# Kernel tuning notes

Hardware: AMD Instinct MI355X
Metric: run time of the kernel (lower is better)

Reference implementation:

```python
import jax, jax.numpy as jnp
import numpy as np

B, T, C, H = 2, 2048, 1024, 16
Dh = C // H  # 64
EPS = 1e-5


def layer_norm(x, g, b):
    mu = jnp.mean(x, axis=-1, keepdims=True)
    var = jnp.mean(jnp.square(x - mu), axis=-1, keepdims=True)
    return (x - mu) * jax.lax.rsqrt(var + EPS) * g + b


def setup_inputs() -> dict:
    key = jax.random.key(0)
    ks = jax.random.split(key, 12)
    s = 0.02
    return {
        "x": jax.random.normal(ks[0], (B, T, C), dtype=jnp.float32),
        # per-head projections, stacked: (H, C, Dh), no bias (bias=False in source)
        "Wq": jax.random.normal(ks[1], (H, C, Dh), dtype=jnp.float32) * s,
        "Wk": jax.random.normal(ks[2], (H, C, Dh), dtype=jnp.float32) * s,
        "Wv": jax.random.normal(ks[3], (H, C, Dh), dtype=jnp.float32) * s,
        "Wo": jax.random.normal(ks[4], (H * Dh, C), dtype=jnp.float32) * s,
        "bo": jnp.zeros((C,), dtype=jnp.float32),
        "W1": jax.random.normal(ks[5], (C, 4 * C), dtype=jnp.float32) * s,
        "b1": jnp.zeros((4 * C,), dtype=jnp.float32),
        "W2": jax.random.normal(ks[6], (4 * C, C), dtype=jnp.float32) * s,
        "b2": jnp.zeros((C,), dtype=jnp.float32),
        "g1": jnp.ones((C,), dtype=jnp.float32),
        "be1": jnp.zeros((C,), dtype=jnp.float32),
        "g2": jnp.ones((C,), dtype=jnp.float32),
        "be2": jnp.zeros((C,), dtype=jnp.float32),
    }


def reference(x, Wq, Wk, Wv, Wo, bo, W1, b1, W2, b2, g1, be1, g2, be2):
    # --- self-attention sublayer ---
    h = layer_norm(x, g1, be1)                       # (B,T,C)
    q = jnp.einsum("btc,hcd->bhtd", h, Wq)
    k = jnp.einsum("btc,hcd->bhtd", h, Wk)
    v = jnp.einsum("btc,hcd->bhtd", h, Wv)
    # NOTE: source scales by C**-0.5 (head INPUT dim), not head_size**-0.5
    scores = jnp.einsum("bhqd,bhkd->bhqk", q, k) * (C ** -0.5)
    # encoder=True default => mask is all ones => no masking applied
    w = jax.nn.softmax(scores, axis=-1)              # (B,H,T,T)
    o = jnp.einsum("bhqk,bhkd->bhqd", w, v)          # (B,H,T,Dh)
    o = o.transpose(0, 2, 1, 3).reshape(B, T, H * Dh)  # concat heads
    attn = o @ Wo + bo                               # output projection
    x = x + attn
    # --- feed-forward sublayer ---
    h2 = layer_norm(x, g2, be2)
    ff = jax.nn.relu(h2 @ W1 + b1) @ W2 + b2
    return x + ff
```

## Files before the change

### kernel.cpp

```cpp
#include <hip/hip_runtime.h>
#include <hip/hip_bf16.h>

#define BT   4096
#define CD   1024
#define TD   2048
#define NH   16
#define DH   64
#define BB   2

typedef __attribute__((ext_vector_type(8))) short bf16x8;
typedef __attribute__((ext_vector_type(4))) short bf16x4;
typedef __attribute__((ext_vector_type(4))) float f32x4;
typedef __attribute__((ext_vector_type(2))) unsigned int u32x2;
typedef __attribute__((ext_vector_type(4))) unsigned int u32x4;

__device__ inline short f2bf(float f) {
    union { float fv; unsigned u; } x; x.fv = f;
    unsigned r = x.u + 0x7fffu + ((x.u >> 16) & 1u);
    return (short)(r >> 16);
}
__device__ inline float bf2f(short s) {
    union { unsigned u; float f; } x; x.u = ((unsigned)(unsigned short)s) << 16;
    return x.f;
}
__device__ inline unsigned pk2bf(float a, float b) {
    union { __hip_bfloat162 h; unsigned u; } cv;
    cv.h = __float22bfloat162_rn(float2{a, b});
    return cv.u;
}

#if __has_builtin(__builtin_amdgcn_exp2f)
#define EXP2(x) __builtin_amdgcn_exp2f(x)
#else
#define EXP2(x) exp2f(x)
#endif

__device__ inline void gload_lds16(const short* g, short* lds) {
    __builtin_amdgcn_global_load_lds(
        (const __attribute__((address_space(1))) void*)g,
        (__attribute__((address_space(3))) void*)lds, 16, 0, 0);
}

__launch_bounds__(256)
__global__ void ln_kernel(const float* __restrict__ x,
                          const float* __restrict__ g,
                          const float* __restrict__ be,
                          short* __restrict__ out) {
    __shared__ float red[2][4];
    const int row = blockIdx.x;
    const int c4 = threadIdx.x * 4;
    const float* xr = x + (size_t)row * CD;
    float4 v = *(const float4*)&xr[c4];
    float s  = (v.x + v.y) + (v.z + v.w);
    float ss = (v.x * v.x + v.y * v.y) + (v.z * v.z + v.w * v.w);
    #pragma unroll
    for (int off = 32; off > 0; off >>= 1) {
        s  += __shfl_down(s,  off, 64);
        ss += __shfl_down(ss, off, 64);
    }
    int wid = threadIdx.x >> 6, lane = threadIdx.x & 63;
    if (lane == 0) { red[0][wid] = s; red[1][wid] = ss; }
    __syncthreads();
    float sum   = red[0][0] + red[0][1] + red[0][2] + red[0][3];
    float sumsq = red[1][0] + red[1][1] + red[1][2] + red[1][3];
    float mu   = sum * (1.f / CD);
    float var  = sumsq * (1.f / CD) - mu * mu;
    float rstd = rsqrtf(var + 1e-5f);
    float4 gv = *(const float4*)&g[c4];
    float4 bv = *(const float4*)&be[c4];
    bf16x4 o;
    o[0] = f2bf((v.x - mu) * rstd * gv.x + bv.x);
    o[1] = f2bf((v.y - mu) * rstd * gv.y + bv.y);
    o[2] = f2bf((v.z - mu) * rstd * gv.z + bv.z);
    o[3] = f2bf((v.w - mu) * rstd * gv.w + bv.w);
    *(bf16x4*)&out[(size_t)row * CD + c4] = o;
}

__launch_bounds__(256)
__global__ void prep_weights(const float* __restrict__ Wq, const float* __restrict__ Wk,
                             const float* __restrict__ Wv, const float* __restrict__ Wo,
                             const float* __restrict__ W1, const float* __restrict__ W2,
                             short* __restrict__ wqt, short* __restrict__ wot,
                             short* __restrict__ w1t, short* __restrict__ w2t) {
    __shared__ float tt[64][65];
    const int id = blockIdx.x;
    const float* in; short* out; int R, Cc, r0, c0;
    if (id < 768) {
        int which = id >> 8, rem = id & 255, hh = rem >> 4, ry = rem & 15;
        in  = (which == 0 ? Wq : which == 1 ? Wk : Wv) + (size_t)hh * CD * DH;
        out = wqt + (size_t)which * CD * CD + (size_t)hh * DH * CD;
        R = CD; Cc = DH; r0 = ry * 64; c0 = 0;
    } else if (id < 1024) {
        int t = id - 768;  in = Wo; out = wot; R = CD;     Cc = CD;     r0 = (t >> 4) * 64; c0 = (t & 15) * 64;
    } else if (id < 2048) {
        int t = id - 1024; in = W1; out = w1t; R = CD;     Cc = 4 * CD; r0 = (t >> 6) * 64; c0 = (t & 63) * 64;
    } else {
        int t = id - 2048; in = W2; out = w2t; R = 4 * CD; Cc = CD;     r0 = (t >> 4) * 64; c0 = (t & 15) * 64;
    }
    const int tid = threadIdx.x;
    #pragma unroll
    for (int i = 0; i < 4; ++i) {
        int f = i * 256 + tid;
        int r = f >> 4, cc = (f & 15) * 4;
        float4 vv = *(const float4*)&in[(size_t)(r0 + r) * Cc + c0 + cc];
        tt[r][cc]     = vv.x;
        tt[r][cc + 1] = vv.y;
        tt[r][cc + 2] = vv.z;
        tt[r][cc + 3] = vv.w;
    }
    __syncthreads();
    #pragma unroll
    for (int i = 0; i < 16; ++i) {
        int e = i * 256 + tid;
        out[(size_t)(c0 + (e >> 6)) * R + r0 + (e & 63)] = f2bf(tt[e & 63][e >> 6]);
    }
}

__launch_bounds__(256)
__global__ void vtrans(const short* __restrict__ vin, short* __restrict__ vout) {
    __shared__ short t[64 * 65];
    const int tid = threadIdx.x;
    const int bh = blockIdx.y;
    const int t0 = blockIdx.x * 64;
    const int b = bh >> 4, h = bh & 15;
    const short* src = vin + (size_t)b * TD * CD + (size_t)h * DH;
    short* dst = vout + (size_t)bh * DH * TD;
    #pragma unroll
    for (int i = 0; i < 16; ++i) {
        int e = i * 256 + tid;
        t[(e >> 6) * 65 + (e & 63)] = src[(size_t)(t0 + (e >> 6)) * CD + (e & 63)];
    }
    __syncthreads();
    #pragma unroll
    for (int i = 0; i < 16; ++i) {
        int e = i * 256 + tid;
        int d = e >> 6, tt = e & 63;
        dst[(size_t)d * TD + t0 + tt] = t[tt * 65 + d];
    }
}

template <int MODE, int TN, int GR>
__launch_bounds__(GR * 256)
__global__ void gemm_mfma(const short* __restrict__ A,
                          const short* __restrict__ Bt,
                          const float* __restrict__ bias,
                          const float* __restrict__ resid,
                          float* __restrict__ outf,
                          short* __restrict__ outb,
                          int N, int K) {
    __shared__ __align__(16) short smem[GR * 3 * (128 + TN) * 32];
    const int tid = threadIdx.x;
    const int kgrp = (GR == 2) ? (tid >> 8) : 0;
    const int tid256 = tid & 255;
    const int w4 = tid256 >> 6, lane = tid & 63;
    const int quad = lane >> 4, l16 = lane & 15;
    const int wr = w4 >> 1, wc = w4 & 1;
    const int li = blockIdx.y * gridDim.x + blockIdx.x;
    const int m0 = ((li & 7) * 4 + ((li >> 3) & 3)) * 128;
    const int n0 = (li >> 5) * TN;
    const int NT = TN / 32;
    const int kbase = kgrp * (K / GR);

    short* grpBase = smem + (size_t)kgrp * 3 * (128 + TN) * 32;
#define AS(bi) (grpBase + (bi) * (128 + TN) * 32)
#define BS(bi) (AS(bi) + 128 * 32)

    f32x4 acc[4][NT] = {};

    auto STAGE = [&](int kt, int bi) {
        const int k0 = kbase + kt * 32;
        short* as = AS(bi);
        short* bs = BS(bi);
        #pragma unroll
        for (int i = 0; i < 2; ++i) {
            int s = i * 256 + tid256;
            int row = s >> 2, kc = (s & 3) ^ ((row >> 1) & 3);
            gload_lds16(A + (size_t)(m0 + row) * K + k0 + kc * 8,
                        &as[(i * 256 + w4 * 64) * 8]);
        }
        #pragma unroll
        for (int i = 0; i < TN / 64; ++i) {
            int s = i * 256 + tid256;
            int row = s >> 2, kc = (s & 3) ^ ((row >> 1) & 3);
            gload_lds16(Bt + (size_t)(n0 + row) * K + k0 + kc * 8,
                        &bs[(i * 256 + w4 * 64) * 8]);
        }
    };

    auto COMPUTE = [&](int bi) {
        const int xo = (quad ^ ((l16 >> 1) & 3)) * 8;
        const short* as = AS(bi);
        const short* bs = BS(bi);
        bf16x8 a[4], b[NT];
        #pragma unroll
        for (int mt = 0; mt < 4; ++mt)
            a[mt] = *(const bf16x8*)&as[(wr * 64 + mt * 16 + l16) * 32 + xo];
        #pragma unroll
        for (int nt = 0; nt < NT; ++nt)
            b[nt] = *(const bf16x8*)&bs[(wc * (TN / 2) + nt * 16 + l16) * 32 + xo];
        #pragma unroll
        for (int mt = 0; mt < 4; ++mt)
            #pragma unroll
            for (int nt = 0; nt < NT; ++nt)
                acc[mt][nt] = __builtin_amdgcn_mfma_f32_16x16x32_bf16(a[mt], b[nt], acc[mt][nt], 0, 0, 0);
    };

    const int nk = (K / GR) >> 5;
    STAGE(0, 0);
    STAGE(1, 1);
    int bi = 0;
    for (int t = 0; t < nk - 1; ++t) {
        asm volatile("s_waitcnt vmcnt(4)" ::: "memory");
        __builtin_amdgcn_s_barrier();
        asm volatile("" ::: "memory");
        int bn = bi + 2 >= 3 ? bi - 1 : bi + 2;
        if (t + 2 < nk) STAGE(t + 2, bn);
        COMPUTE(bi);
        bi = bi + 1 >= 3 ? 0 : bi + 1;
    }
    asm volatile("s_waitcnt vmcnt(0)" ::: "memory");
    __builtin_amdgcn_s_barrier();
    asm volatile("" ::: "memory");
    COMPUTE(bi);

    if (GR == 2) {
        float* red = (float*)smem;
        __syncthreads();
        if (kgrp == 1) {
            #pragma unroll
            for (int mt = 0; mt < 4; ++mt)
                #pragma unroll
                for (int nt = 0; nt < NT; ++nt)
                    *(f32x4*)&red[((mt * NT + nt) * 256 + w4 * 64 + lane) * 4] = acc[mt][nt];
        }
        __syncthreads();
        if (kgrp == 1) return;
        #pragma unroll
        for (int mt = 0; mt < 4; ++mt)
            #pragma unroll
            for (int nt = 0; nt < NT; ++nt) {
                f32x4 p = *(const f32x4*)&red[((mt * NT + nt) * 256 + w4 * 64 + lane) * 4];
                acc[mt][nt] += p;
            }
    }

    const float qsc = (MODE == 5 && n0 < CD) ? 0.03125f * 1.44269504f : 1.0f;
    short* ob5 = (MODE == 5) ? outb + (size_t)(n0 >> 10) * BT * CD : nullptr;

    #pragma unroll
    for (int mt = 0; mt < 4; ++mt)
        #pragma unroll
        for (int nt = 0; nt < NT; ++nt)
            #pragma unroll
            for (int reg = 0; reg < 4; ++reg) {
                int row = m0 + wr * 64 + mt * 16 + quad * 4 + reg;
                int col = n0 + wc * (TN / 2) + nt * 16 + l16;
                float v = acc[mt][nt][reg];
                if (MODE == 1) { v += bias[col] + resid[(size_t)row * N + col];
                                 outf[(size_t)row * N + col] = v; }
                if (MODE == 2) { v = fmaxf(v + bias[col], 0.f);
                                 outb[(size_t)row * N + col] = f2bf(v); }
                if (MODE == 5) { ob5[(size_t)row * CD + (col & 1023)] = f2bf(v * qsc); }
            }
#undef AS
#undef BS
}

#define BQ   128
#define BK   64
#define STR  68

__launch_bounds__(256)
__global__ void attn_mfma(const short* __restrict__ q,
                          const short* __restrict__ k,
                          const short* __restrict__ vt,
                          short* __restrict__ opart,
                          float* __restrict__ lpart) {
    __shared__ short Ks[2][BK * STR];
    __shared__ short Vt[2][DH * STR];

    const int tid  = threadIdx.x;
    const int w = tid >> 6, lane = tid & 63;
    const int quad = lane >> 4, l16 = lane & 15;
    const int h = blockIdx.y;
    const int b = blockIdx.z >> 1, split = blockIdx.z & 1;
    const int q0 = blockIdx.x * BQ;
    const size_t base  = (size_t)b * TD * CD + (size_t)h * DH;
    const size_t vbase = (size_t)(b * NH + h) * DH * TD;

    bf16x8 qf[2][2];
    #pragma unroll
    for (int rt = 0; rt < 2; ++rt) {
        const short* qp = q + base + (size_t)(q0 + w * 32 + rt * 16 + l16) * CD;
        qf[rt][0] = *(const bf16x8*)&qp[quad * 8];
        qf[rt][1] = *(const bf16x8*)&qp[32 + quad * 8];
    }

    const bf16x8 ones = {(short)0x3F80, (short)0x3F80, (short)0x3F80, (short)0x3F80,
                         (short)0x3F80, (short)0x3F80, (short)0x3F80, (short)0x3F80};
    f32x4 O_l[2] = {};
    f32x4 O[2][4] = {};

    const int kbeg = split * (TD / 2);
    const int NTI = (TD / 2) / BK;

    const int r8 = tid >> 3, c8 = (tid & 7) * 8;
    const int s32 = ((r8 & 4) << 2) + ((r8 >> 3) << 2) + (r8 & 3);
    const short* kg = k + base + c8;
    const short* vg = vt + vbase + (size_t)r8 * TD + c8;

#define ISSUE_T(t, K0, K1, V0, V1) do {                                   \
        const size_t ko_ = (size_t)(kbeg + (t) * BK);                     \
        K0 = *(const bf16x8*)&kg[(ko_ + r8) * CD];                        \
        K1 = *(const bf16x8*)&kg[(ko_ + r8 + 32) * CD];                   \
        V0 = *(const bf16x8*)&vg[ko_];                                    \
        V1 = *(const bf16x8*)&vg[(size_t)32 * TD + ko_];                  \
    } while (0)

#define WRITE_T(buf, K0, K1, V0, V1) do {                                 \
        *(bf16x8*)&Ks[buf][s32 * STR + c8] = K0;                          \
        *(bf16x8*)&Ks[buf][(s32 + 32) * STR + c8] = K1;                   \
        *(bf16x8*)&Vt[buf][r8 * STR + c8] = V0;                           \
        *(bf16x8*)&Vt[buf][(r8 + 32) * STR + c8] = V1;                    \
    } while (0)

#define COMPUTE_T(buf) do {                                               \
        __builtin_amdgcn_s_setprio(1);                                    \
        _Pragma("unroll")                                                 \
        for (int sp = 0; sp < 2; ++sp) {                                  \
            bf16x8 kbe0 = *(const bf16x8*)&Ks[buf][(sp * 32 + l16) * STR + quad * 8];      \
            bf16x8 kbe1 = *(const bf16x8*)&Ks[buf][(sp * 32 + l16) * STR + 32 + quad * 8]; \
            bf16x8 kbo0 = *(const bf16x8*)&Ks[buf][(sp * 32 + 16 + l16) * STR + quad * 8]; \
            bf16x8 kbo1 = *(const bf16x8*)&Ks[buf][(sp * 32 + 16 + l16) * STR + 32 + quad * 8]; \
            bf16x8 pa8[2];                                                \
            _Pragma("unroll")                                             \
            for (int rt = 0; rt < 2; ++rt) {                              \
                f32x4 ae = (f32x4){0.f, 0.f, 0.f, 0.f};                   \
                f32x4 ao = (f32x4){0.f, 0.f, 0.f, 0.f};                   \
                ae = __builtin_amdgcn_mfma_f32_16x16x32_bf16(kbe0, qf[rt][0], ae, 0, 0, 0); \
                ae = __builtin_amdgcn_mfma_f32_16x16x32_bf16(kbe1, qf[rt][1], ae, 0, 0, 0); \
                ao = __builtin_amdgcn_mfma_f32_16x16x32_bf16(kbo0, qf[rt][0], ao, 0, 0, 0); \
                ao = __builtin_amdgcn_mfma_f32_16x16x32_bf16(kbo1, qf[rt][1], ao, 0, 0, 0); \
                float pe0 = EXP2(ae[0]), pe1 = EXP2(ae[1]);               \
                float pe2 = EXP2(ae[2]), pe3 = EXP2(ae[3]);               \
                float po0 = EXP2(ao[0]), po1 = EXP2(ao[1]);               \
                float po2 = EXP2(ao[2]), po3 = EXP2(ao[3]);               \
                union { u32x4 u; bf16x8 s; } cv_;                         \
                cv_.u = (u32x4){pk2bf(pe0, pe1), pk2bf(pe2, pe3),         \
                                pk2bf(po0, po1), pk2bf(po2, po3)};        \
                pa8[rt] = cv_.s;                                          \
            }                                                             \
            _Pragma("unroll")                                             \
            for (int dt = 0; dt < 4; ++dt) {                              \
                bf16x8 vb = *(const bf16x8*)&Vt[buf][(dt * 16 + l16) * STR + sp * 32 + quad * 8]; \
                O[0][dt] = __builtin_amdgcn_mfma_f32_16x16x32_bf16(pa8[0], vb, O[0][dt], 0, 0, 0); \
                O[1][dt] = __builtin_amdgcn_mfma_f32_16x16x32_bf16(pa8[1], vb, O[1][dt], 0, 0, 0); \
            }                                                             \
            O_l[0] = __builtin_amdgcn_mfma_f32_16x16x32_bf16(pa8[0], ones, O_l[0], 0, 0, 0); \
            O_l[1] = __builtin_amdgcn_mfma_f32_16x16x32_bf16(pa8[1], ones, O_l[1], 0, 0, 0); \
        }                                                                 \
        __builtin_amdgcn_s_setprio(0);                                    \
    } while (0)

    bf16x8 kA0, kA1, vA0, vA1;
    bf16x8 kB0, kB1, vB0, vB1;

    ISSUE_T(0, kA0, kA1, vA0, vA1);
    WRITE_T(0, kA0, kA1, vA0, vA1);
    ISSUE_T(1, kA0, kA1, vA0, vA1);
    __syncthreads();

    for (int it = 0; it < NTI; it += 2) {
        if (it + 2 < NTI) ISSUE_T(it + 2, kB0, kB1, vB0, vB1);
        COMPUTE_T(0);
        WRITE_T(1, kA0, kA1, vA0, vA1);
        __syncthreads();
        if (it + 3 < NTI) ISSUE_T(it + 3, kA0, kA1, vA0, vA1);
        COMPUTE_T(1);
        if (it + 2 < NTI) WRITE_T(0, kB0, kB1, vB0, vB1);
        __syncthreads();
    }
#undef ISSUE_T
#undef WRITE_T
#undef COMPUTE_T

    short* osp = opart + (size_t)split * BT * CD;
    float* lsp = lpart + (size_t)split * BB * NH * TD + (size_t)(b * NH + h) * TD;
    #pragma unroll
    for (int rt = 0; rt < 2; ++rt) {
        if (l16 == 0)
            *(f32x4*)&lsp[q0 + w * 32 + rt * 16 + quad * 4] = O_l[rt];
        #pragma unroll
        for (int reg = 0; reg < 4; ++reg) {
            int row = q0 + w * 32 + rt * 16 + quad * 4 + reg;
            short* op = osp + base + (size_t)row * CD;
            #pragma unroll
            for (int dt = 0; dt < 4; ++dt)
                op[dt * 16 + l16] = f2bf(O[rt][dt][reg]);
        }
    }
}

__launch_bounds__(256)
__global__ void attn_combine(const short* __restrict__ opart,
                             const float* __restrict__ lpart,
                             short* __restrict__ ob) {
    const size_t idx = ((size_t)blockIdx.x * 256 + threadIdx.x) * 8;
    const int row = (int)(idx >> 10);
    const int col = (int)(idx & 1023);
    const int b = row >> 11, qq = row & (TD - 1), hh = col >> 6;
    const size_t lbase = (size_t)(b * NH + hh) * TD + qq;
    const float l0 = lpart[lbase];
    const float l1 = lpart[(size_t)BB * NH * TD + lbase];
    const float inv = 1.f / (l0 + l1);
    bf16x8 a = *(const bf16x8*)&opart[idx];
    bf16x8 c = *(const bf16x8*)&opart[(size_t)BT * CD + idx];
    bf16x8 r;
    #pragma unroll
    for (int j = 0; j < 8; ++j)
        r[j] = f2bf((bf2f(a[j]) + bf2f(c[j])) * inv);
    *(bf16x8*)&ob[idx] = r;
}

extern "C" void kernel_launch(void* const* d_in, const int* in_sizes, int n_in,
                              void* d_out, int out_size, void* d_ws, size_t ws_size,
                              hipStream_t stream) {
    const float* x   = (const float*)d_in[0];
    const float* Wq  = (const float*)d_in[1];
    const float* Wk  = (const float*)d_in[2];
    const float* Wv  = (const float*)d_in[3];
    const float* Wo  = (const float*)d_in[4];
    const float* bo  = (const float*)d_in[5];
    const float* W1  = (const float*)d_in[6];
    const float* b1  = (const float*)d_in[7];
    const float* W2  = (const float*)d_in[8];
    const float* b2  = (const float*)d_in[9];
    const float* g1  = (const float*)d_in[10];
    const float* be1 = (const float*)d_in[11];
    const float* g2  = (const float*)d_in[12];
    const float* be2 = (const float*)d_in[13];
    float* out = (float*)d_out;

    const size_t SZ = (size_t)BT * CD;
    float* ws  = (float*)d_ws;
    short* qbf = (short*)ws;
    short* kbf = qbf + SZ;
    short* vbf = qbf + 2 * SZ;
    float* lpart = ws + SZ + SZ / 2;
    short* opart = (short*)(ws + 2 * SZ);
    float* x1  = ws + 2 * SZ;
    short* h   = (short*)(ws + 3 * SZ);
    short* ob  = (short*)(ws + 3 * SZ + SZ / 2);
    short* wqt = (short*)(ws + 4 * SZ);
    short* wot = wqt + 3 * CD * CD;
    short* w1t = (short*)(ws + 4 * SZ + SZ / 2);
    short* w2t = (short*)(ws + 5 * SZ);
    short* vtg = (short*)(ws + 5 * SZ + SZ / 2);
    short* ff1 = (short*)ws;

    ln_kernel<<<BT, 256, 0, stream>>>(x, g1, be1, h);

    prep_weights<<<3072, 256, 0, stream>>>(Wq, Wk, Wv, Wo, W1, W2, wqt, wot, w1t, w2t);

    gemm_mfma<5, 128, 1><<<dim3(24, 32), 256, 0, stream>>>(h, wqt, nullptr, nullptr, nullptr, qbf, 3 * CD, CD);

    vtrans<<<dim3(TD / 64, 2 * NH), 256, 0, stream>>>(vbf, vtg);

    attn_mfma<<<dim3(TD / BQ, NH, BB * 2), 256, 0, stream>>>(qbf, kbf, vtg, opart, lpart);

    attn_combine<<<dim3((int)(SZ / (256 * 8))), 256, 0, stream>>>(opart, lpart, ob);

    gemm_mfma<1, 128, 2><<<dim3(8, 32), 512, 0, stream>>>(ob, wot, bo, x, x1, nullptr, CD, CD);

    ln_kernel<<<BT, 256, 0, stream>>>(x1, g2, be2, h);

    gemm_mfma<2, 128, 1><<<dim3(32, 32), 256, 0, stream>>>(h, w1t, b1, nullptr, nullptr, ff1, 4 * CD, CD);

    gemm_mfma<1, 128, 2><<<dim3(8, 32), 512, 0, stream>>>(ff1, w2t, b2, x1, out, nullptr, CD, 4 * CD);
}
```

Measured before the change: 317.9 us.

## Stage attention K/V tiles via direct global-to-LDS loads with triple buffering

The attention kernel now copies K and V tiles straight from global memory into LDS with direct-to-LDS loads, instead of loading into registers and then writing to LDS. It uses three 32-key buffers with vmcnt-based waits, so two tiles are in flight while one is computed. Bank conflicts are avoided with an XOR swizzle rather than row padding. The aim is lower register pressure and VGPR round trips, allowing higher occupancy (launch bounds of 5 waves), and more overlap of memory latency with compute. The cost is a barrier per smaller tile, which adds more synchronisation.

```diff
diff --git a/kernel.cpp b/kernel.cpp
--- a/kernel.cpp
+++ b/kernel.cpp
@@ -267,17 +267,16 @@
 }
 
 #define BQ   128
-#define BK   64
-#define STR  68
-
-__launch_bounds__(256)
+#define BK   32
+
+__launch_bounds__(256, 5)
 __global__ void attn_mfma(const short* __restrict__ q,
                           const short* __restrict__ k,
                           const short* __restrict__ vt,
                           short* __restrict__ opart,
                           float* __restrict__ lpart) {
-    __shared__ short Ks[2][BK * STR];
-    __shared__ short Vt[2][DH * STR];
+    __shared__ short Ks[3][BK * DH];
+    __shared__ short Vt[3][DH * BK];
 
     const int tid  = threadIdx.x;
     const int w = tid >> 6, lane = tid & 63;
@@ -304,84 +303,74 @@
     const int kbeg = split * (TD / 2);
     const int NTI = (TD / 2) / BK;
 
-    const int r8 = tid >> 3, c8 = (tid & 7) * 8;
-    const int s32 = ((r8 & 4) << 2) + ((r8 >> 3) << 2) + (r8 & 3);
-    const short* kg = k + base + c8;
-    const short* vg = vt + vbase + (size_t)r8 * TD + c8;
-
-#define ISSUE_T(t, K0, K1, V0, V1) do {                                   \
-        const size_t ko_ = (size_t)(kbeg + (t) * BK);                     \
-        K0 = *(const bf16x8*)&kg[(ko_ + r8) * CD];                        \
-        K1 = *(const bf16x8*)&kg[(ko_ + r8 + 32) * CD];                   \
-        V0 = *(const bf16x8*)&vg[ko_];                                    \
-        V1 = *(const bf16x8*)&vg[(size_t)32 * TD + ko_];                  \
+    const int ks  = tid >> 3;
+    const int kc  = (tid & 7) ^ (ks & 7);
+    const int kkey = (((ks & 15) >> 2) << 3) + (ks & 3) + ((ks >> 4) << 2);
+    const short* kgp = k + base + (size_t)kkey * CD + kc * 8;
+    const int vd = tid >> 2;
+    const int vc = (tid & 3) ^ ((vd >> 1) & 3);
+    const short* vgp = vt + vbase + (size_t)vd * TD + vc * 8;
+
+#define STAGE_T(kt, bi) do {                                              \
+        const size_t ko_ = (size_t)(kbeg + (kt) * BK);                    \
+        gload_lds16(kgp + ko_ * CD, &Ks[bi][w * 512]);                    \
+        gload_lds16(vgp + ko_,      &Vt[bi][w * 512]);                    \
     } while (0)
 
-#define WRITE_T(buf, K0, K1, V0, V1) do {                                 \
-        *(bf16x8*)&Ks[buf][s32 * STR + c8] = K0;                          \
-        *(bf16x8*)&Ks[buf][(s32 + 32) * STR + c8] = K1;                   \
-        *(bf16x8*)&Vt[buf][r8 * STR + c8] = V0;                           \
-        *(bf16x8*)&Vt[buf][(r8 + 32) * STR + c8] = V1;                    \
-    } while (0)
-
-#define COMPUTE_T(buf) do {                                               \
+#define COMPUTE_T(bi) do {                                                \
         __builtin_amdgcn_s_setprio(1);                                    \
+        const int kswz = l16 & 7;                                         \
+        bf16x8 kbe0 = *(const bf16x8*)&Ks[bi][l16 * 64 + ((quad) ^ kswz) * 8];        \
+        bf16x8 kbe1 = *(const bf16x8*)&Ks[bi][l16 * 64 + ((4 + quad) ^ kswz) * 8];    \
+        bf16x8 kbo0 = *(const bf16x8*)&Ks[bi][(16 + l16) * 64 + ((quad) ^ kswz) * 8]; \
+        bf16x8 kbo1 = *(const bf16x8*)&Ks[bi][(16 + l16) * 64 + ((4 + quad) ^ kswz) * 8]; \
+        bf16x8 pa8[2];                                                    \
         _Pragma("unroll")                                                 \
-        for (int sp = 0; sp < 2; ++sp) {                                  \
-            bf16x8 kbe0 = *(const bf16x8*)&Ks[buf][(sp * 32 + l16) * STR + quad * 8];      \
-            bf16x8 kbe1 = *(const bf16x8*)&Ks[buf][(sp * 32 + l16) * STR + 32 + quad * 8]; \
-            bf16x8 kbo0 = *(const bf16x8*)&Ks[buf][(sp * 32 + 16 + l16) * STR + quad * 8]; \
-            bf16x8 kbo1 = *(const bf16x8*)&Ks[buf][(sp * 32 + 16 + l16) * STR + 32 + quad * 8]; \
-            bf16x8 pa8[2];                                                \
-            _Pragma("unroll")                                             \
-            for (int rt = 0; rt < 2; ++rt) {                              \
-                f32x4 ae = (f32x4){0.f, 0.f, 0.f, 0.f};                   \
-                f32x4 ao = (f32x4){0.f, 0.f, 0.f, 0.f};                   \
-                ae = __builtin_amdgcn_mfma_f32_16x16x32_bf16(kbe0, qf[rt][0], ae, 0, 0, 0); \
-                ae = __builtin_amdgcn_mfma_f32_16x16x32_bf16(kbe1, qf[rt][1], ae, 0, 0, 0); \
-                ao = __builtin_amdgcn_mfma_f32_16x16x32_bf16(kbo0, qf[rt][0], ao, 0, 0, 0); \
-                ao = __builtin_amdgcn_mfma_f32_16x16x32_bf16(kbo1, qf[rt][1], ao, 0, 0, 0); \
-                float pe0 = EXP2(ae[0]), pe1 = EXP2(ae[1]);               \
-                float pe2 = EXP2(ae[2]), pe3 = EXP2(ae[3]);               \
-                float po0 = EXP2(ao[0]), po1 = EXP2(ao[1]);               \
-                float po2 = EXP2(ao[2]), po3 = EXP2(ao[3]);               \
-                union { u32x4 u; bf16x8 s; } cv_;                         \
-                cv_.u = (u32x4){pk2bf(pe0, pe1), pk2bf(pe2, pe3),         \
-                                pk2bf(po0, po1), pk2bf(po2, po3)};        \
-                pa8[rt] = cv_.s;                                          \
-            }                                                             \
-            _Pragma("unroll")                                             \
-            for (int dt = 0; dt < 4; ++dt) {                              \
-                bf16x8 vb = *(const bf16x8*)&Vt[buf][(dt * 16 + l16) * STR + sp * 32 + quad * 8]; \
-                O[0][dt] = __builtin_amdgcn_mfma_f32_16x16x32_bf16(pa8[0], vb, O[0][dt], 0, 0, 0); \
-                O[1][dt] = __builtin_amdgcn_mfma_f32_16x16x32_bf16(pa8[1], vb, O[1][dt], 0, 0, 0); \
-            }                                                             \
-            O_l[0] = __builtin_amdgcn_mfma_f32_16x16x32_bf16(pa8[0], ones, O_l[0], 0, 0, 0); \
-            O_l[1] = __builtin_amdgcn_mfma_f32_16x16x32_bf16(pa8[1], ones, O_l[1], 0, 0, 0); \
+        for (int rt = 0; rt < 2; ++rt) {                                  \
+            f32x4 ae = (f32x4){0.f, 0.f, 0.f, 0.f};                       \
+            f32x4 ao = (f32x4){0.f, 0.f, 0.f, 0.f};                       \
+            ae = __builtin_amdgcn_mfma_f32_16x16x32_bf16(kbe0, qf[rt][0], ae, 0, 0, 0); \
+            ae = __builtin_amdgcn_mfma_f32_16x16x32_bf16(kbe1, qf[rt][1], ae, 0, 0, 0); \
+            ao = __builtin_amdgcn_mfma_f32_16x16x32_bf16(kbo0, qf[rt][0], ao, 0, 0, 0); \
+            ao = __builtin_amdgcn_mfma_f32_16x16x32_bf16(kbo1, qf[rt][1], ao, 0, 0, 0); \
+            float pe0 = EXP2(ae[0]), pe1 = EXP2(ae[1]);                   \
+            float pe2 = EXP2(ae[2]), pe3 = EXP2(ae[3]);                   \
+            float po0 = EXP2(ao[0]), po1 = EXP2(ao[1]);                   \
+            float po2 = EXP2(ao[2]), po3 = EXP2(ao[3]);                   \
+            union { u32x4 u; bf16x8 s; } cv_;                             \
+            cv_.u = (u32x4){pk2bf(pe0, pe1), pk2bf(pe2, pe3),             \
+                            pk2bf(po0, po1), pk2bf(po2, po3)};            \
+            pa8[rt] = cv_.s;                                              \
         }                                                                 \
+        const int vswz = (l16 >> 1) & 3;                                  \
+        _Pragma("unroll")                                                 \
+        for (int dt = 0; dt < 4; ++dt) {                                  \
+            bf16x8 vb = *(const bf16x8*)&Vt[bi][(dt * 16 + l16) * 32 + ((quad) ^ vswz) * 8]; \
+            O[0][dt] = __builtin_amdgcn_mfma_f32_16x16x32_bf16(pa8[0], vb, O[0][dt], 0, 0, 0); \
+            O[1][dt] = __builtin_amdgcn_mfma_f32_16x16x32_bf16(pa8[1], vb, O[1][dt], 0, 0, 0); \
+        }                                                                 \
+        O_l[0] = __builtin_amdgcn_mfma_f32_16x16x32_bf16(pa8[0], ones, O_l[0], 0, 0, 0); \
+        O_l[1] = __builtin_amdgcn_mfma_f32_16x16x32_bf16(pa8[1], ones, O_l[1], 0, 0, 0); \
         __builtin_amdgcn_s_setprio(0);                                    \
     } while (0)
 
-    bf16x8 kA0, kA1, vA0, vA1;
-    bf16x8 kB0, kB1, vB0, vB1;
-
-    ISSUE_T(0, kA0, kA1, vA0, vA1);
-    WRITE_T(0, kA0, kA1, vA0, vA1);
-    ISSUE_T(1, kA0, kA1, vA0, vA1);
-    __syncthreads();
-
-    for (int it = 0; it < NTI; it += 2) {
-        if (it + 2 < NTI) ISSUE_T(it + 2, kB0, kB1, vB0, vB1);
-        COMPUTE_T(0);
-        WRITE_T(1, kA0, kA1, vA0, vA1);
-        __syncthreads();
-        if (it + 3 < NTI) ISSUE_T(it + 3, kA0, kA1, vA0, vA1);
-        COMPUTE_T(1);
-        if (it + 2 < NTI) WRITE_T(0, kB0, kB1, vB0, vB1);
-        __syncthreads();
-    }
-#undef ISSUE_T
-#undef WRITE_T
+    STAGE_T(0, 0);
+    STAGE_T(1, 1);
+    int bi = 0;
+    for (int t = 0; t < NTI - 1; ++t) {
+        asm volatile("s_waitcnt vmcnt(2)" ::: "memory");
+        __builtin_amdgcn_s_barrier();
+        asm volatile("" ::: "memory");
+        int bn = bi + 2 >= 3 ? bi - 1 : bi + 2;
+        if (t + 2 < NTI) STAGE_T(t + 2, bn);
+        COMPUTE_T(bi);
+        bi = bi + 1 >= 3 ? 0 : bi + 1;
+    }
+    asm volatile("s_waitcnt vmcnt(0)" ::: "memory");
+    __builtin_amdgcn_s_barrier();
+    asm volatile("" ::: "memory");
+    COMPUTE_T(bi);
+#undef STAGE_T
 #undef COMPUTE_T
 
     short* osp = opart + (size_t)split * BT * CD;
```

Result: no change. 318.4 us (+0.1%).
